# Performance work log

Hardware: AMD Instinct MI355X
Metric: run time of the kernel (lower is better)

## Reference

```python
import jax, jax.numpy as jnp
import numpy as np

N, T = 2000, 8
INFEAT, HID, OUT, H = 32, 16, 32, 4
ALPHA = 0.2
D1 = HID * H   # 64, layer-1 GRU dim (concat heads)
D2 = OUT       # 32, layer-2 GRU dim (mean heads)
NEG = -1e9


def setup_inputs() -> dict:
    key = jax.random.key(0)
    ks = jax.random.split(key, 12)
    xav = lambda k, shape, fi, fo: (jax.random.normal(k, shape, dtype=jnp.float32)
                                    * np.float32(np.sqrt(2.0 / (fi + fo))))
    # sparse-ish binary adjacency with self loops, per timestep
    A = (jax.random.uniform(ks[0], (T, N, N)) < 0.01).astype(jnp.float32)
    A = jnp.maximum(A, jnp.eye(N, dtype=jnp.float32)[None])
    feats = jax.random.normal(ks[1], (T, N, INFEAT), dtype=jnp.float32) * 0.1
    return {
        "A": A,
        "feats": feats,
        "gat1_W": xav(ks[2], (H, INFEAT, HID), INFEAT, HID),
        "gat1_a": xav(ks[3], (H, 2, HID), 2 * HID, 1),
        "gru1_W": xav(ks[4], (3, N, D1, D1), D1, D1),
        "gru1_U": xav(ks[5], (3, N, D1, D1), D1, D1),
        "gru1_b": jnp.zeros((3, N, D1), jnp.float32),
        "q1": xav(ks[6], (N, D1), N, D1),   # GAT_init_features, layer 1
        "gat2_W": xav(ks[7], (H, D1, OUT), D1, OUT),
        "gat2_a": xav(ks[8], (H, 2, OUT), 2 * OUT, 1),
        "gru2_W": xav(ks[9], (3, N, D2, D2), D2, D2),
        "gru2_U": xav(ks[10], (3, N, D2, D2), D2, D2),
        "gru2_b": jnp.zeros((3, N, D2), jnp.float32),
        "q2": xav(ks[11], (N, D2), N, D2),  # GAT_init_features, layer 2
    }


def _gat(x, At, W, a, concat):
    # x: [N,F], At: [N,N], W: [H,F,D], a: [H,2,D]
    h = jnp.einsum('nf,hfd->hnd', x, W)                       # [H,N,D]
    e_src = jnp.einsum('hnd,hd->hn', h, a[:, 0])              # [H,N]
    e_dst = jnp.einsum('hnd,hd->hn', h, a[:, 1])
    e = jax.nn.leaky_relu(e_src[:, :, None] + e_dst[:, None, :], ALPHA)
    e = jnp.where(At[None] > 0, e, NEG)
    att = jax.nn.softmax(e, axis=-1)                          # [H,N,N]
    o = jnp.einsum('hnm,hmd->hnd', att, h)
    if concat:
        return jax.nn.elu(o).transpose(1, 0, 2).reshape(x.shape[0], -1)  # [N,H*D]
    return o.mean(axis=0)                                     # [N,D]


def _gru_step(Q, Z, Wg, Ug, bg):
    # batched per-node mat_GRU_cell: Wg/Ug [3,N,D,D], bg [3,N,D]; gates: update, reset, htilda
    wz = jnp.einsum('gnij,nj->gni', Wg, Z) + bg               # [3,N,D]
    upd = jax.nn.sigmoid(wz[0] + jnp.einsum('nij,nj->ni', Ug[0], Q))
    rst = jax.nn.sigmoid(wz[1] + jnp.einsum('nij,nj->ni', Ug[1], Q))
    hcap = jnp.tanh(wz[2] + jnp.einsum('nij,nj->ni', Ug[2], rst * Q))
    return (1.0 - upd) * Q + upd * hcap


def _grcu_layer(A, feats, q0, W, a, Wg, Ug, bg, concat):
    def step(Q, inp):
        At, xt = inp
        Z = _gat(xt, At, W, a, concat)
        Qn = _gru_step(Q, Z, Wg, Ug, bg)
        return Qn, Qn
    _, seq = jax.lax.scan(step, q0, (A, feats))
    return seq  # [T,N,Dim]


def reference(A, feats, gat1_W, gat1_a, gru1_W, gru1_U, gru1_b, q1,
              gat2_W, gat2_a, gru2_W, gru2_U, gru2_b, q2):
    s1 = _grcu_layer(A, feats, q1, gat1_W, gat1_a, gru1_W, gru1_U, gru1_b, True)
    s2 = _grcu_layer(A, s1, q2, gat2_W, gat2_a, gru2_W, gru2_U, gru2_b, False)
    return s2.reshape(-1, s2.shape[-1])  # torch.cat(out_seq, dim=0) -> [T*N, OUT]
```

## Files before the change

### kernel.cpp

```cpp
#include <hip/hip_runtime.h>
#include <cstdint>
#include <cstddef>

#define NNODES 2000
#define TSTEPS 8
#define NHEADS 4
#define CAP    96
#define NROWS  (TSTEPS * NNODES)

__global__ void k1_csr_gath1(const float* __restrict__ A,
                             int* __restrict__ nbr, int* __restrict__ cnt,
                             const float* __restrict__ feats,
                             const float* __restrict__ W, const float* __restrict__ a,
                             float* __restrict__ hbuf, float* __restrict__ es,
                             float* __restrict__ ed) {
    const int lane = threadIdx.x;
    if (blockIdx.x < NROWS) {
        const int row = blockIdx.x;
        const float* Ar = A + (size_t)row * NNODES;
        int* outp = nbr + (size_t)row * CAP;
        int c = 0;
        for (int j0 = 0; j0 < NNODES; j0 += 64) {
            int j = j0 + lane;
            bool p = (j < NNODES) && (Ar[j] > 0.0f);
            unsigned long long m = __ballot(p);
            int off = __popcll(m & ((1ull << lane) - 1ull));
            if (p) { int pos = c + off; if (pos < CAP) outp[pos] = j; }
            c += (int)__popcll(m);
        }
        if (lane == 0) cnt[row] = (c > CAP ? CAP : c);
    } else {
        const int b = blockIdx.x - NROWS;
        const int t = b / NNODES, n = b % NNODES;
        constexpr int F = 32, D = 16;
        const int h = lane / D, d = lane % D;
        const float* xr = feats + (size_t)b * F;
        const float* Wp = W + (size_t)h * F * D + d;
        float acc = 0.f;
        #pragma unroll
        for (int f = 0; f < F; ++f) acc += xr[f] * Wp[f * D];
        hbuf[(((size_t)t * NHEADS + h) * NNODES + n) * D + d] = acc;
        float s0 = acc * a[(h * 2 + 0) * D + d];
        float s1 = acc * a[(h * 2 + 1) * D + d];
        #pragma unroll
        for (int s = D / 2; s > 0; s >>= 1) {
            s0 += __shfl_down(s0, s, D);
            s1 += __shfl_down(s1, s, D);
        }
        if (d == 0) {
            es[((size_t)t * NHEADS + h) * NNODES + n] = s0;
            ed[((size_t)t * NHEADS + h) * NNODES + n] = s1;
        }
    }
}

template<int F, int D>
__global__ void gat_h_all_kernel(const float* __restrict__ x, const float* __restrict__ W,
                                 const float* __restrict__ a, float* __restrict__ hbuf,
                                 float* __restrict__ es, float* __restrict__ ed) {
    const int b = blockIdx.x;
    const int t = b / NNODES, n = b % NNODES;
    const int tid = threadIdx.x;
    const int h = tid / D, d = tid % D;
    const float* xr = x + (size_t)b * F;
    const float* Wp = W + (size_t)h * F * D + d;
    float acc = 0.f;
    #pragma unroll
    for (int f = 0; f < F; ++f) acc += xr[f] * Wp[f * D];
    hbuf[(((size_t)t * NHEADS + h) * NNODES + n) * D + d] = acc;
    float s0 = acc * a[(h * 2 + 0) * D + d];
    float s1 = acc * a[(h * 2 + 1) * D + d];
    #pragma unroll
    for (int s = D / 2; s > 0; s >>= 1) {
        s0 += __shfl_down(s0, s, D);
        s1 += __shfl_down(s1, s, D);
    }
    if (d == 0) {
        es[((size_t)t * NHEADS + h) * NNODES + n] = s0;
        ed[((size_t)t * NHEADS + h) * NNODES + n] = s1;
    }
}

template<int D, bool CONCAT>
__global__ void gat_attn_all_kernel(const int* __restrict__ nbr, const int* __restrict__ cnt_arr,
                                    const float* __restrict__ hbuf, const float* __restrict__ es,
                                    const float* __restrict__ ed, float* __restrict__ Z) {
    const int b = blockIdx.x;
    const int t = b / NNODES, n = b % NNODES;
    const int tid = threadIdx.x;
    const int h = tid / D, d = tid % D;
    const int cnt = cnt_arr[b];
    const int* idx = nbr + (size_t)b * CAP;
    const float* esb = es + (size_t)t * NHEADS * NNODES;
    const float* edb = ed + (size_t)t * NHEADS * NNODES;
    const float* hb  = hbuf + (size_t)t * NHEADS * NNODES * D;
    __shared__ int mlist[CAP];
    __shared__ float eds[NHEADS][CAP];
    for (int k = tid; k < cnt; k += NHEADS * D) mlist[k] = idx[k];
    __syncthreads();
    for (int k = d; k < cnt; k += D) eds[h][k] = edb[(size_t)h * NNODES + mlist[k]];
    __syncthreads();
    const float esv = esb[(size_t)h * NNODES + n];
    float maxv = -1e30f;
    for (int k = 0; k < cnt; ++k) {
        float v = esv + eds[h][k];
        v = v > 0.f ? v : 0.2f * v;
        maxv = fmaxf(maxv, v);
    }
    float wsum = 0.f, acc = 0.f;
    for (int k = 0; k < cnt; ++k) {
        float v = esv + eds[h][k];
        v = v > 0.f ? v : 0.2f * v;
        float w = __expf(v - maxv);
        wsum += w;
        acc += w * hb[((size_t)h * NNODES + mlist[k]) * D + d];
    }
    float o = acc / wsum;
    if constexpr (CONCAT) {
        float e = o > 0.f ? o : (__expf(o) - 1.0f);
        Z[(size_t)b * (NHEADS * D) + h * D + d] = e;
    } else {
        __shared__ float red[NHEADS][D];
        red[h][d] = o;
        __syncthreads();
        if (h == 0) Z[(size_t)b * D + d] =
            (red[0][d] + red[1][d] + red[2][d] + red[3][d]) * 0.25f;
    }
}

template<int D>
__global__ void wzgru_kernel(const float* __restrict__ Wg, const float* __restrict__ Ug,
                             const float* __restrict__ bg, const float* __restrict__ Z,
                             const float* __restrict__ q0, float* __restrict__ outp) {
    constexpr int QUADS = D / 16;
    constexpr int TPB = QUADS * D;
    const int n = blockIdx.x, tid = threadIdx.x;
    const int quad = tid & (QUADS - 1);
    const int row  = tid / QUADS;
    const int cbase = quad * 16;
    __shared__ float Zs[TSTEPS][D];
    __shared__ float wzs[3][TSTEPS][D];
    __shared__ float Qs[D], rq[D];

    for (int idx = tid; idx < TSTEPS * D / 4; idx += TPB) {
        int t = idx / (D / 4), i4 = idx % (D / 4);
        reinterpret_cast<float4*>(&Zs[t][0])[i4] =
            reinterpret_cast<const float4*>(Z + ((size_t)t * NNODES + n) * D)[i4];
    }
    if (tid < D) Qs[tid] = q0[(size_t)n * D + tid];
    float bgv[3];
    #pragma unroll
    for (int g = 0; g < 3; ++g) bgv[g] = bg[((size_t)g * NNODES + n) * D + row];
    float wseg[3][16];
    #pragma unroll
    for (int g = 0; g < 3; ++g) {
        const float4* W4 = reinterpret_cast<const float4*>(
            Wg + ((size_t)g * NNODES + n) * D * D + (size_t)row * D + cbase);
        #pragma unroll
        for (int c = 0; c < 4; ++c) {
            float4 v = W4[c];
            wseg[g][c * 4 + 0] = v.x; wseg[g][c * 4 + 1] = v.y;
            wseg[g][c * 4 + 2] = v.z; wseg[g][c * 4 + 3] = v.w;
        }
    }
    __syncthreads();

    #pragma unroll
    for (int t = 0; t < TSTEPS; ++t) {
        float z16[16];
        #pragma unroll
        for (int c = 0; c < 4; ++c) {
            float4 v = reinterpret_cast<const float4*>(&Zs[t][cbase])[c];
            z16[c * 4 + 0] = v.x; z16[c * 4 + 1] = v.y;
            z16[c * 4 + 2] = v.z; z16[c * 4 + 3] = v.w;
        }
        #pragma unroll
        for (int g = 0; g < 3; ++g) {
            float p = 0.f;
            #pragma unroll
            for (int c = 0; c < 16; ++c) p += wseg[g][c] * z16[c];
            if constexpr (QUADS == 4) { p += __shfl_xor(p, 1, 4); p += __shfl_xor(p, 2, 4); }
            else                      { p += __shfl_xor(p, 1, 2); }
            if (quad == 0) wzs[g][t][row] = p + bgv[g];
        }
    }

    float useg[3][16];
    #pragma unroll
    for (int g = 0; g < 3; ++g) {
        const float4* U4 = reinterpret_cast<const float4*>(
            Ug + ((size_t)g * NNODES + n) * D * D + (size_t)row * D + cbase);
        #pragma unroll
        for (int c = 0; c < 4; ++c) {
            float4 v = U4[c];
            useg[g][c * 4 + 0] = v.x; useg[g][c * 4 + 1] = v.y;
            useg[g][c * 4 + 2] = v.z; useg[g][c * 4 + 3] = v.w;
        }
    }
    __syncthreads();

    for (int t = 0; t < TSTEPS; ++t) {
        float q16[16];
        #pragma unroll
        for (int c = 0; c < 4; ++c) {
            float4 v = reinterpret_cast<const float4*>(&Qs[cbase])[c];
            q16[c * 4 + 0] = v.x; q16[c * 4 + 1] = v.y;
            q16[c * 4 + 2] = v.z; q16[c * 4 + 3] = v.w;
        }
        float p0 = 0.f, p1 = 0.f;
        #pragma unroll
        for (int c = 0; c < 16; ++c) { p0 += useg[0][c] * q16[c]; p1 += useg[1][c] * q16[c]; }
        if constexpr (QUADS == 4) {
            p0 += __shfl_xor(p0, 1, 4); p0 += __shfl_xor(p0, 2, 4);
            p1 += __shfl_xor(p1, 1, 4); p1 += __shfl_xor(p1, 2, 4);
        } else {
            p0 += __shfl_xor(p0, 1, 2); p1 += __shfl_xor(p1, 1, 2);
        }
        const float qrow = Qs[row];
        const float zg = 1.f / (1.f + __expf(-(wzs[0][t][row] + p0)));
        const float rg = 1.f / (1.f + __expf(-(wzs[1][t][row] + p1)));
        if (quad == 0) rq[row] = rg * qrow;
        __syncthreads();
        float p2 = 0.f;
        {
            float r16[16];
            #pragma unroll
            for (int c = 0; c < 4; ++c) {
                float4 v = reinterpret_cast<const float4*>(&rq[cbase])[c];
                r16[c * 4 + 0] = v.x; r16[c * 4 + 1] = v.y;
                r16[c * 4 + 2] = v.z; r16[c * 4 + 3] = v.w;
            }
            #pragma unroll
            for (int c = 0; c < 16; ++c) p2 += useg[2][c] * r16[c];
        }
        if constexpr (QUADS == 4) { p2 += __shfl_xor(p2, 1, 4); p2 += __shfl_xor(p2, 2, 4); }
        else                      { p2 += __shfl_xor(p2, 1, 2); }
        const float hcap = tanhf(wzs[2][t][row] + p2);
        const float qn = (1.f - zg) * qrow + zg * hcap;
        if (quad == 0) {
            Qs[row] = qn;
            outp[((size_t)t * NNODES + n) * D + row] = qn;
        }
        __syncthreads();
    }
}

extern "C" void kernel_launch(void* const* d_in, const int* in_sizes, int n_in,
                              void* d_out, int out_size, void* d_ws, size_t ws_size,
                              hipStream_t stream) {
    const float* A      = (const float*)d_in[0];
    const float* feats  = (const float*)d_in[1];
    const float* gat1_W = (const float*)d_in[2];
    const float* gat1_a = (const float*)d_in[3];
    const float* gru1_W = (const float*)d_in[4];
    const float* gru1_U = (const float*)d_in[5];
    const float* gru1_b = (const float*)d_in[6];
    const float* q1     = (const float*)d_in[7];
    const float* gat2_W = (const float*)d_in[8];
    const float* gat2_a = (const float*)d_in[9];
    const float* gru2_W = (const float*)d_in[10];
    const float* gru2_U = (const float*)d_in[11];
    const float* gru2_b = (const float*)d_in[12];
    const float* q2     = (const float*)d_in[13];
    float* out = (float*)d_out;

    char* ws = (char*)d_ws;
    int*   nbr  = (int*)ws;    ws += (size_t)NROWS * CAP * 4;
    int*   cnt  = (int*)ws;    ws += (size_t)NROWS * 4;
    float* h1   = (float*)ws;  ws += (size_t)TSTEPS * NHEADS * NNODES * 16 * 4;
    float* es1  = (float*)ws;  ws += (size_t)TSTEPS * NHEADS * NNODES * 4;
    float* ed1  = (float*)ws;  ws += (size_t)TSTEPS * NHEADS * NNODES * 4;
    float* Z1   = (float*)ws;  ws += (size_t)TSTEPS * NNODES * 64 * 4;
    float* s1   = (float*)ws;  ws += (size_t)TSTEPS * NNODES * 64 * 4;
    float* h2   = (float*)ws;  ws += (size_t)TSTEPS * NHEADS * NNODES * 32 * 4;
    float* es2  = (float*)ws;  ws += (size_t)TSTEPS * NHEADS * NNODES * 4;
    float* ed2  = (float*)ws;  ws += (size_t)TSTEPS * NHEADS * NNODES * 4;
    float* Z2   = (float*)ws;  ws += (size_t)TSTEPS * NNODES * 32 * 4;

    k1_csr_gath1<<<2 * NROWS, 64, 0, stream>>>(A, nbr, cnt, feats, gat1_W, gat1_a,
                                               h1, es1, ed1);
    gat_attn_all_kernel<16, true><<<NROWS, 64, 0, stream>>>(nbr, cnt, h1, es1, ed1, Z1);
    wzgru_kernel<64><<<NNODES, 256, 0, stream>>>(gru1_W, gru1_U, gru1_b, Z1, q1, s1);
    gat_h_all_kernel<64, 32><<<NROWS, 128, 0, stream>>>(s1, gat2_W, gat2_a, h2, es2, ed2);
    gat_attn_all_kernel<32, false><<<NROWS, 128, 0, stream>>>(nbr, cnt, h2, es2, ed2, Z2);
    wzgru_kernel<32><<<NNODES, 64, 0, stream>>>(gru2_W, gru2_U, gru2_b, Z2, q2, out);
}
```

Before: 186.8 us.

## Stage GRU weight matrices through padded LDS with coalesced double-buffered loads

The GRU kernel now loads each per-node W and U gate matrix with fully coalesced float4 reads (consecutive threads read consecutive float4s) into registers, writes them to a padded double-buffered shared-memory tile, and reads each thread's row segment back from LDS. The next matrix's global load is issued before the current one is consumed, so memory traffic overlaps with compute. The CSR build kernel also switches to float4 reads of the adjacency row, running four ballots per load. The cost is extra LDS traffic, more barriers, and higher register pressure from holding prefetch buffers.

```diff
diff --git a/kernel.cpp b/kernel.cpp
--- a/kernel.cpp
+++ b/kernel.cpp
@@ -17,16 +17,21 @@
     const int lane = threadIdx.x;
     if (blockIdx.x < NROWS) {
         const int row = blockIdx.x;
-        const float* Ar = A + (size_t)row * NNODES;
+        const float4* Ar4 = reinterpret_cast<const float4*>(A + (size_t)row * NNODES);
         int* outp = nbr + (size_t)row * CAP;
+        const unsigned long long lmask = (1ull << lane) - 1ull;
         int c = 0;
-        for (int j0 = 0; j0 < NNODES; j0 += 64) {
-            int j = j0 + lane;
-            bool p = (j < NNODES) && (Ar[j] > 0.0f);
-            unsigned long long m = __ballot(p);
-            int off = __popcll(m & ((1ull << lane) - 1ull));
-            if (p) { int pos = c + off; if (pos < CAP) outp[pos] = j; }
-            c += (int)__popcll(m);
+        for (int j4 = lane; j4 < NNODES / 4; j4 += 64) {
+            float4 v = Ar4[j4];
+            #pragma unroll
+            for (int cc = 0; cc < 4; ++cc) {
+                float x = (cc == 0) ? v.x : (cc == 1) ? v.y : (cc == 2) ? v.z : v.w;
+                bool p = x > 0.0f;
+                unsigned long long m = __ballot(p);
+                int off = __popcll(m & lmask);
+                if (p && c + off < CAP) outp[c + off] = j4 * 4 + cc;
+                c += (int)__popcll(m);
+            }
         }
         if (lane == 0) cnt[row] = (c > CAP ? CAP : c);
     } else {
@@ -134,16 +139,49 @@
                              const float* __restrict__ q0, float* __restrict__ outp) {
     constexpr int QUADS = D / 16;
     constexpr int TPB = QUADS * D;
+    constexpr int F4R = D / 4;
+    constexpr int PF4R = F4R + 1;
     const int n = blockIdx.x, tid = threadIdx.x;
     const int quad = tid & (QUADS - 1);
     const int row  = tid / QUADS;
     const int cbase = quad * 16;
+    __shared__ float4 sbuf[2][D * PF4R];
     __shared__ float Zs[TSTEPS][D];
     __shared__ float wzs[3][TSTEPS][D];
     __shared__ float Qs[D], rq[D];
 
+    const float4* mats[6];
+    #pragma unroll
+    for (int g = 0; g < 3; ++g) {
+        mats[g]     = reinterpret_cast<const float4*>(Wg + ((size_t)g * NNODES + n) * D * D);
+        mats[g + 3] = reinterpret_cast<const float4*>(Ug + ((size_t)g * NNODES + n) * D * D);
+    }
+    auto gload = [&](float4* r, const float4* m) {
+        #pragma unroll
+        for (int k = 0; k < 4; ++k) r[k] = m[k * TPB + tid];
+    };
+    auto swrite = [&](int bi, const float4* r) {
+        #pragma unroll
+        for (int k = 0; k < 4; ++k) {
+            int j = k * TPB + tid;
+            sbuf[bi][(j / F4R) * PF4R + (j % F4R)] = r[k];
+        }
+    };
+    auto sread = [&](int bi, float* seg) {
+        #pragma unroll
+        for (int c = 0; c < 4; ++c) {
+            float4 v = sbuf[bi][row * PF4R + quad * 4 + c];
+            seg[c * 4 + 0] = v.x; seg[c * 4 + 1] = v.y;
+            seg[c * 4 + 2] = v.z; seg[c * 4 + 3] = v.w;
+        }
+    };
+
+    float4 ra[4], rb[4];
+    gload(ra, mats[0]);
+    gload(rb, mats[1]);
+
     for (int idx = tid; idx < TSTEPS * D / 4; idx += TPB) {
-        int t = idx / (D / 4), i4 = idx % (D / 4);
+        int t = idx / F4R, i4 = idx % F4R;
         reinterpret_cast<float4*>(&Zs[t][0])[i4] =
             reinterpret_cast<const float4*>(Z + ((size_t)t * NNODES + n) * D)[i4];
     }
@@ -151,19 +189,11 @@
     float bgv[3];
     #pragma unroll
     for (int g = 0; g < 3; ++g) bgv[g] = bg[((size_t)g * NNODES + n) * D + row];
-    float wseg[3][16];
-    #pragma unroll
-    for (int g = 0; g < 3; ++g) {
-        const float4* W4 = reinterpret_cast<const float4*>(
-            Wg + ((size_t)g * NNODES + n) * D * D + (size_t)row * D + cbase);
-        #pragma unroll
-        for (int c = 0; c < 4; ++c) {
-            float4 v = W4[c];
-            wseg[g][c * 4 + 0] = v.x; wseg[g][c * 4 + 1] = v.y;
-            wseg[g][c * 4 + 2] = v.z; wseg[g][c * 4 + 3] = v.w;
-        }
-    }
-    __syncthreads();
+
+    float wseg[3][16], useg[3][16];
+    swrite(0, ra); gload(ra, mats[2]); __syncthreads(); sread(0, wseg[0]);
+    swrite(1, rb); gload(rb, mats[3]); __syncthreads(); sread(1, wseg[1]);
+    swrite(0, ra); gload(ra, mats[4]); __syncthreads(); sread(0, wseg[2]);
 
     #pragma unroll
     for (int t = 0; t < TSTEPS; ++t) {
@@ -185,19 +215,9 @@
         }
     }
 
-    float useg[3][16];
-    #pragma unroll
-    for (int g = 0; g < 3; ++g) {
-        const float4* U4 = reinterpret_cast<const float4*>(
-            Ug + ((size_t)g * NNODES + n) * D * D + (size_t)row * D + cbase);
-        #pragma unroll
-        for (int c = 0; c < 4; ++c) {
-            float4 v = U4[c];
-            useg[g][c * 4 + 0] = v.x; useg[g][c * 4 + 1] = v.y;
-            useg[g][c * 4 + 2] = v.z; useg[g][c * 4 + 3] = v.w;
-        }
-    }
-    __syncthreads();
+    swrite(1, rb); gload(rb, mats[5]); __syncthreads(); sread(1, useg[0]);
+    swrite(0, ra);                     __syncthreads(); sread(0, useg[1]);
+    swrite(1, rb);                     __syncthreads(); sread(1, useg[2]);
 
     for (int t = 0; t < TSTEPS; ++t) {
         float q16[16];
```

Result: slower. 267.4 us (+43.2%).
